# Kernel optimization log

Hardware: AMD Instinct MI355X
Metric: run time of the kernel (lower is better)

## Reference

```python
import jax, jax.numpy as jnp
import numpy as np

DIM = 512
NUM_GROUPS = 32
NUM_HEADS = 8
EPS = 1e-5


def group_norm(x, gamma, beta):
    # x: (B, C, H, W); normalize over (C//G, H, W) per group
    B, C, H, W = x.shape
    g = x.reshape(B, NUM_GROUPS, -1)
    mean = g.mean(axis=2, keepdims=True)
    var = g.var(axis=2, keepdims=True)
    g = (g - mean) * jax.lax.rsqrt(var + EPS)
    x = g.reshape(B, C, H, W)
    return x * gamma[None, :, None, None] + beta[None, :, None, None]


def setup_inputs() -> dict:
    key = jax.random.key(0)
    ks = jax.random.split(key, 7)
    B, C, H, W = 16, DIM, 32, 32
    x = jax.random.normal(ks[0], (B, C, H, W), dtype=jnp.float32)
    gamma = jnp.ones((C,), dtype=jnp.float32)
    beta = jnp.zeros((C,), dtype=jnp.float32)
    s_in = 1.0 / np.sqrt(C)
    w_qkv = jax.random.normal(ks[1], (3 * C, C), dtype=jnp.float32) * s_in
    b_qkv = jnp.zeros((3 * C,), dtype=jnp.float32)
    w_proj = jax.random.normal(ks[2], (C, C), dtype=jnp.float32) * s_in
    b_proj = jnp.zeros((C,), dtype=jnp.float32)
    return {"x": x, "gamma": gamma, "beta": beta, "w_qkv": w_qkv,
            "b_qkv": b_qkv, "w_proj": w_proj, "b_proj": b_proj}


def reference(x, gamma, beta, w_qkv, b_qkv, w_proj, b_proj):
    B, C, H, W = x.shape
    nh = NUM_HEADS
    c3 = 3 * C // nh          # per-head qkv channels (3 * head_dim)
    dh = C // nh              # head_dim
    scale = C ** (-0.5)       # NOTE: source scales by full dim, not head_dim

    h = group_norm(x, gamma, beta)

    # 1x1 conv qkv projection: (B, 3C, H, W)
    qkv = jnp.einsum('bchw,oc->bohw', h, w_qkv) + b_qkv[None, :, None, None]

    # rearrange 'b (head c) h w -> (b head) (h w) c'
    qkv = qkv.reshape(B, nh, c3, H, W)
    qkv = qkv.transpose(0, 1, 3, 4, 2).reshape(B * nh, H * W, c3)
    q, k, v = jnp.split(qkv, 3, axis=2)   # each (B*nh, HW, dh)

    score = jnp.einsum('bnc,bmc->bnm', q, k * scale)   # (B*nh, HW, HW)
    attn = jax.nn.softmax(score, axis=2)
    out = jnp.einsum('bnm,bmc->bnc', attn, v)          # (B*nh, HW, dh)

    # rearrange '(head b) (h w) c -> b (head c) h w'  (NOTE head-major, as in source)
    out = out.reshape(nh, B, H, W, dh)
    out = out.transpose(1, 0, 4, 2, 3).reshape(B, C, H, W)

    out = jnp.einsum('bchw,oc->bohw', out, w_proj) + b_proj[None, :, None, None]
    return out + x
```

## Files before the change

kernel.cpp:

```cpp
#include <hip/hip_runtime.h>
#include <stdint.h>

typedef __bf16 bf16;
typedef __attribute__((ext_vector_type(4))) float f32x4;
typedef __attribute__((ext_vector_type(8))) __bf16 bf16x8;
typedef __attribute__((ext_vector_type(4))) __bf16 bf16x4;

#define NB 16
#define CH 512
#define HWS 1024
#define NHEAD 8
#define DH 64
#define O3 1536
#define CPQ 136
#define CPF 132

#define PSW(row, col) (((row) << 6) + (((((col) >> 3) ^ ((row) & 7))) << 3) + ((col) & 7))

__device__ __forceinline__ void gload_lds16(const bf16* g, bf16* l) {
    __builtin_amdgcn_global_load_lds(
        (const __attribute__((address_space(1))) unsigned int*)g,
        (__attribute__((address_space(3))) unsigned int*)l,
        16, 0, 0);
}

#if defined(__has_builtin) && __has_builtin(__builtin_amdgcn_exp2f)
__device__ __forceinline__ float fast_exp2(float x) { return __builtin_amdgcn_exp2f(x); }
#else
__device__ __forceinline__ float fast_exp2(float x) { return exp2f(x); }
#endif

__global__ void prep(const float* __restrict__ x, float* __restrict__ stats,
                     const float* __restrict__ wq, const float* __restrict__ wp,
                     bf16* __restrict__ wq_b, bf16* __restrict__ wp_b) {
    int bx = blockIdx.x;
    if (bx < 512) {
        int b = bx >> 5, g = bx & 31;
        const float4* p = (const float4*)(x + ((size_t)(b * CH + g * 16)) * HWS);
        float s = 0.f, ss = 0.f;
        for (int i = threadIdx.x; i < 4096; i += 256) {
            float4 v = p[i];
            s  += v.x + v.y + v.z + v.w;
            ss += v.x*v.x + v.y*v.y + v.z*v.z + v.w*v.w;
        }
        for (int off = 32; off; off >>= 1) {
            s  += __shfl_xor(s,  off, 64);
            ss += __shfl_xor(ss, off, 64);
        }
        __shared__ float red[8];
        int w = threadIdx.x >> 6;
        if ((threadIdx.x & 63) == 0) { red[w*2] = s; red[w*2+1] = ss; }
        __syncthreads();
        if (threadIdx.x == 0) {
            float S  = red[0] + red[2] + red[4] + red[6];
            float SS = red[1] + red[3] + red[5] + red[7];
            float mean = S * (1.f/16384.f);
            float var  = SS * (1.f/16384.f) - mean*mean;
            stats[bx*2]   = mean;
            stats[bx*2+1] = rsqrtf(var + 1e-5f);
        }
    } else {
        int i = (bx - 512) * 256 + threadIdx.x;
        if (i < O3*CH) wq_b[i] = (bf16)wq[i];
        else           wp_b[i - O3*CH] = (bf16)wp[i - O3*CH];
    }
}

__global__ void gn_apply_t(const float* __restrict__ x, const float* __restrict__ stats,
                           const float* __restrict__ gamma, const float* __restrict__ beta,
                           bf16* __restrict__ hT) {
    __shared__ float tile[32][33];
    int bx = blockIdx.x;
    int b = bx >> 9;
    int rem = bx & 511;
    int ct = rem >> 5, nt = rem & 31;
    int tx = threadIdx.x & 31, ty = threadIdx.x >> 5;
    #pragma unroll
    for (int r = 0; r < 4; ++r) {
        int c = ct*32 + ty + r*8;
        int n = nt*32 + tx;
        float v = x[((size_t)(b * CH + c)) * HWS + n];
        int g = c >> 4;
        float mean = stats[(b*32+g)*2], rstd = stats[(b*32+g)*2+1];
        tile[ty + r*8][tx] = (v - mean) * rstd * gamma[c] + beta[c];
    }
    __syncthreads();
    #pragma unroll
    for (int r = 0; r < 4; ++r) {
        int n = nt*32 + ty + r*8;
        int c = ct*32 + tx;
        hT[((size_t)(b * HWS + n)) * CH + c] = (bf16)tile[tx][ty + r*8];
    }
}

__global__ __launch_bounds__(256, 3)
void qkv_gemm(const bf16* __restrict__ W, const bf16* __restrict__ hT,
              const float* __restrict__ bias, bf16* __restrict__ qkv,
              bf16* __restrict__ vT) {
    __shared__ __align__(16) bf16 SMEM[128*CPQ];
    bf16* As = SMEM;
    bf16* Bs = SMEM + 8192;
    int bx = blockIdx.x;
    int po = bx >> 7, qo = bx & 127;
    int obase = po*128, bnbase = qo*128;
    int tid = threadIdx.x;
    int lane = tid & 63, w = tid >> 6;
    int quad = lane >> 4, l15 = lane & 15;
    int wm = w >> 1, wn = w & 1;
    int x7 = l15 & 7;
    int srow = lane >> 3, spos = lane & 7;
    int sgc = (spos ^ srow) * 8;

    f32x4 acc[4][4] = {};
    for (int k0 = 0; k0 < 512; k0 += 64) {
        #pragma unroll
        for (int r = 0; r < 4; ++r) {
            int rb = r*32 + w*8;
            gload_lds16(W  + ((size_t)(obase  + rb + srow))*512 + k0 + sgc, &As[rb*64]);
            gload_lds16(hT + ((size_t)(bnbase + rb + srow))*512 + k0 + sgc, &Bs[rb*64]);
        }
        __syncthreads();
        #pragma unroll
        for (int ks = 0; ks < 2; ++ks) {
            int ch = (ks*4 + quad) ^ x7;
            bf16x8 af[4], bfv[4];
            #pragma unroll
            for (int mt = 0; mt < 4; ++mt)
                af[mt] = *(const bf16x8*)(&As[(wm*64 + mt*16 + l15)*64 + ch*8]);
            #pragma unroll
            for (int nt = 0; nt < 4; ++nt)
                bfv[nt] = *(const bf16x8*)(&Bs[(wn*64 + nt*16 + l15)*64 + ch*8]);
            #pragma unroll
            for (int mt = 0; mt < 4; ++mt)
                #pragma unroll
                for (int nt = 0; nt < 4; ++nt)
                    acc[mt][nt] = __builtin_amdgcn_mfma_f32_16x16x32_bf16(af[mt], bfv[nt], acc[mt][nt], 0, 0, 0);
        }
        __syncthreads();
    }

    bf16* Cs = SMEM;
    int b = bnbase >> 10;
    int nbase = bnbase & 1023;
    #pragma unroll
    for (int mt = 0; mt < 4; ++mt) {
        int o0 = obase + wm*64 + mt*16 + quad*4;
        float4 bb = *(const float4*)(bias + o0);
        int c192 = o0 % 192;
        bool isV = (c192 >= 128);
        int h = o0 / 192;
        int d0 = c192 - 128;
        #pragma unroll
        for (int nt = 0; nt < 4; ++nt) {
            int bn_l = wn*64 + nt*16 + l15;
            bf16x4 v;
            v[0] = (bf16)(acc[mt][nt][0] + bb.x);
            v[1] = (bf16)(acc[mt][nt][1] + bb.y);
            v[2] = (bf16)(acc[mt][nt][2] + bb.z);
            v[3] = (bf16)(acc[mt][nt][3] + bb.w);
            *(bf16x4*)(&Cs[bn_l*CPQ + (o0 - obase)]) = v;
            if (isV) {
                int key = nbase + bn_l;
                size_t vb_ = ((size_t)((b*8 + h)*64 + d0)) * HWS + key;
                vT[vb_]          = v[0];
                vT[vb_ + HWS]    = v[1];
                vT[vb_ + 2*HWS]  = v[2];
                vT[vb_ + 3*HWS]  = v[3];
            }
        }
    }
    __syncthreads();
    #pragma unroll
    for (int p = 0; p < 8; ++p) {
        int bn_l = p*16 + (tid >> 4);
        int o8 = (tid & 15) * 8;
        if ((obase + o8) % 192 < 128) {
            uint4 v = *(const uint4*)(&Cs[bn_l*CPQ + o8]);
            *(uint4*)(qkv + ((size_t)(bnbase + bn_l)) * O3 + obase + o8) = v;
        }
    }
}

__global__ __launch_bounds__(512, 4)
void flash_attn(const bf16* __restrict__ qkv, const bf16* __restrict__ vT,
                bf16* __restrict__ A2) {
    __shared__ __align__(16) bf16 Ks[2][64*64];
    __shared__ __align__(16) bf16 Vs[2][64*64];
    __shared__ __align__(16) bf16 Ps[8][32*64];
    int bx = blockIdx.x;
    int g = bx & 127, qt = bx >> 7;
    int b = g >> 3, h = g & 7;
    int tid = threadIdx.x, lane = tid & 63, w = tid >> 6;
    int quad = lane >> 4, l15 = lane & 15;
    int x7 = l15 & 7;
    int srow = lane >> 3, spos = lane & 7;
    int sgc = (spos ^ srow) * 8;
    const float kLog2 = 0.04419417382415922f * 1.44269504088896341f;

    bf16x8 aq[2][2];
    #pragma unroll
    for (int mt = 0; mt < 2; ++mt) {
        int qrow = qt*256 + w*32 + mt*16 + l15;
        const bf16* qb = qkv + ((size_t)(b * HWS + qrow)) * O3 + h*192;
        aq[mt][0] = *(const bf16x8*)(qb + quad*8);
        aq[mt][1] = *(const bf16x8*)(qb + 32 + quad*8);
        #pragma unroll
        for (int j = 0; j < 8; ++j) {
            aq[mt][0][j] = (bf16)((float)aq[mt][0][j] * kLog2);
            aq[mt][1][j] = (bf16)((float)aq[mt][1][j] * kLog2);
        }
    }

    const bf16* kg = qkv + ((size_t)(b*HWS + w*8 + srow))*O3 + h*192 + 64 + sgc;
    const bf16* vg = vT  + ((size_t)(g*DH  + w*8 + srow))*HWS + sgc;

    gload_lds16(kg, &Ks[0][w*512]);
    gload_lds16(vg, &Vs[0][w*512]);

    f32x4 acc[2][4] = {};
    f32x4 L4[2] = {};
    __syncthreads();

    for (int kt = 0; kt < 16; ++kt) {
        int cur = kt & 1;
        if (kt < 15) {
            gload_lds16(kg + ((size_t)((kt+1)*64))*O3, &Ks[cur^1][w*512]);
            gload_lds16(vg + (kt+1)*64,                &Vs[cur^1][w*512]);
        }
        const bf16* Kc = &Ks[cur][0];
        const bf16* Vc = &Vs[cur][0];

        #pragma unroll
        for (int nt = 0; nt < 4; ++nt) {
            bf16x8 ak0 = *(const bf16x8*)(&Kc[(nt*16 + l15)*64 + ((quad     ^ x7)*8)]);
            bf16x8 ak1 = *(const bf16x8*)(&Kc[(nt*16 + l15)*64 + (((quad+4) ^ x7)*8)]);
            #pragma unroll
            for (int mt = 0; mt < 2; ++mt) {
                f32x4 z = {};
                z = __builtin_amdgcn_mfma_f32_16x16x32_bf16(ak0, aq[mt][0], z, 0, 0, 0);
                z = __builtin_amdgcn_mfma_f32_16x16x32_bf16(ak1, aq[mt][1], z, 0, 0, 0);
                bf16x4 p;
                #pragma unroll
                for (int r = 0; r < 4; ++r) {
                    float e = fast_exp2(z[r]);
                    L4[mt][r] += e;
                    p[r] = (bf16)e;
                }
                *(bf16x4*)(&Ps[w][PSW(mt*16 + l15, nt*16 + quad*4)]) = p;
            }
        }
        bf16x8 ap[2][2];
        #pragma unroll
        for (int mt = 0; mt < 2; ++mt) {
            ap[mt][0] = *(const bf16x8*)(&Ps[w][PSW(mt*16 + l15, quad*8)]);
            ap[mt][1] = *(const bf16x8*)(&Ps[w][PSW(mt*16 + l15, 32 + quad*8)]);
        }
        #pragma unroll
        for (int dt = 0; dt < 4; ++dt) {
            bf16x8 bv0 = *(const bf16x8*)(&Vc[(dt*16 + l15)*64 + ((quad     ^ x7)*8)]);
            bf16x8 bv1 = *(const bf16x8*)(&Vc[(dt*16 + l15)*64 + (((quad+4) ^ x7)*8)]);
            #pragma unroll
            for (int mt = 0; mt < 2; ++mt) {
                acc[mt][dt] = __builtin_amdgcn_mfma_f32_16x16x32_bf16(ap[mt][0], bv0, acc[mt][dt], 0, 0, 0);
                acc[mt][dt] = __builtin_amdgcn_mfma_f32_16x16x32_bf16(ap[mt][1], bv1, acc[mt][dt], 0, 0, 0);
            }
        }
        __syncthreads();
    }

    float Linv[2][4];
    #pragma unroll
    for (int mt = 0; mt < 2; ++mt) {
        float Lf = (L4[mt][0] + L4[mt][1]) + (L4[mt][2] + L4[mt][3]);
        Lf += __shfl_xor(Lf, 16, 64);
        Lf += __shfl_xor(Lf, 32, 64);
        #pragma unroll
        for (int r = 0; r < 4; ++r)
            Linv[mt][r] = 1.f / __shfl(Lf, quad*4 + r, 64);
    }

    #pragma unroll
    for (int mt = 0; mt < 2; ++mt)
        #pragma unroll
        for (int dt = 0; dt < 4; ++dt)
            #pragma unroll
            for (int r = 0; r < 4; ++r)
                Ps[w][PSW(mt*16 + quad*4 + r, dt*16 + l15)] = (bf16)(acc[mt][dt][r] * Linv[mt][r]);

    int bp = g & 15;
    int hp = g >> 4;
    #pragma unroll
    for (int cc = 0; cc < 4; ++cc) {
        int c = cc*64 + lane;
        int row = c >> 3, dcc = c & 7;
        uint4 v = *(const uint4*)(&Ps[w][PSW(row, dcc*8)]);
        size_t idx = ((size_t)(bp * HWS + qt*256 + w*32 + row)) * CH + hp*64 + dcc*8;
        *(uint4*)(A2 + idx) = v;
    }
}

__global__ __launch_bounds__(256, 3)
void proj_gemm(const bf16* __restrict__ A2, const bf16* __restrict__ Wp,
               const float* __restrict__ bias, const float* __restrict__ x,
               float* __restrict__ out) {
    __shared__ __align__(16) bf16 SMEM[16896];
    bf16* As = SMEM;
    bf16* Bs = SMEM + 8192;
    int bx = blockIdx.x;
    int po = bx >> 7, qo = bx & 127;
    int obase = po*128, bnbase = qo*128;
    int tid = threadIdx.x;
    int lane = tid & 63, w = tid >> 6;
    int quad = lane >> 4, l15 = lane & 15;
    int wm = w >> 1, wn = w & 1;
    int x7 = l15 & 7;
    int srow = lane >> 3, spos = lane & 7;
    int sgc = (spos ^ srow) * 8;

    f32x4 acc[4][4] = {};
    for (int k0 = 0; k0 < 512; k0 += 64) {
        #pragma unroll
        for (int r = 0; r < 4; ++r) {
            int rb = r*32 + w*8;
            gload_lds16(A2 + ((size_t)(bnbase + rb + srow))*512 + k0 + sgc, &As[rb*64]);
            gload_lds16(Wp + ((size_t)(obase  + rb + srow))*512 + k0 + sgc, &Bs[rb*64]);
        }
        __syncthreads();
        #pragma unroll
        for (int ks = 0; ks < 2; ++ks) {
            int ch = (ks*4 + quad) ^ x7;
            bf16x8 af[4], bfv[4];
            #pragma unroll
            for (int mt = 0; mt < 4; ++mt)
                af[mt] = *(const bf16x8*)(&As[(wm*64 + mt*16 + l15)*64 + ch*8]);
            #pragma unroll
            for (int nt = 0; nt < 4; ++nt)
                bfv[nt] = *(const bf16x8*)(&Bs[(wn*64 + nt*16 + l15)*64 + ch*8]);
            #pragma unroll
            for (int mt = 0; mt < 4; ++mt)
                #pragma unroll
                for (int nt = 0; nt < 4; ++nt)
                    acc[mt][nt] = __builtin_amdgcn_mfma_f32_16x16x32_bf16(af[mt], bfv[nt], acc[mt][nt], 0, 0, 0);
        }
        __syncthreads();
    }

    float* Cf = (float*)SMEM;
    int bb = bnbase >> 10;
    int nbase = bnbase & 1023;
    #pragma unroll
    for (int hh = 0; hh < 2; ++hh) {
        if (wm == hh) {
            #pragma unroll
            for (int mt = 0; mt < 4; ++mt)
                #pragma unroll
                for (int nt = 0; nt < 4; ++nt)
                    #pragma unroll
                    for (int r = 0; r < 4; ++r)
                        Cf[(mt*16 + quad*4 + r)*CPF + wn*64 + nt*16 + l15] = acc[mt][nt][r];
        }
        __syncthreads();
        #pragma unroll
        for (int p = 0; p < 4; ++p) {
            int ol = p*32 + (tid >> 3);
            int nl0 = (tid & 7) * 8;
            int o = obase + ol;
            float bv = bias[o];
            #pragma unroll
            for (int jj = 0; jj < 2; ++jj) {
                int nl = nl0 + jj*4;
                size_t idx = ((size_t)(bb * CH + o)) * HWS + nbase + hh*64 + nl;
                float4 xr = *(const float4*)(x + idx);
                float4 res;
                res.x = Cf[(nl+0)*CPF + ol] + bv + xr.x;
                res.y = Cf[(nl+1)*CPF + ol] + bv + xr.y;
                res.z = Cf[(nl+2)*CPF + ol] + bv + xr.z;
                res.w = Cf[(nl+3)*CPF + ol] + bv + xr.w;
                *(float4*)(out + idx) = res;
            }
        }
        __syncthreads();
    }
}

extern "C" void kernel_launch(void* const* d_in, const int* in_sizes, int n_in,
                              void* d_out, int out_size, void* d_ws, size_t ws_size,
                              hipStream_t stream) {
    const float* x      = (const float*)d_in[0];
    const float* gamma  = (const float*)d_in[1];
    const float* beta   = (const float*)d_in[2];
    const float* w_qkv  = (const float*)d_in[3];
    const float* b_qkv  = (const float*)d_in[4];
    const float* w_proj = (const float*)d_in[5];
    const float* b_proj = (const float*)d_in[6];
    float* out = (float*)d_out;

    char* ws = (char*)d_ws;
    float* stats = (float*)(ws + 0);
    bf16*  wq_b  = (bf16*)(ws + 4096);
    bf16*  wp_b  = (bf16*)(ws + 1576960);
    bf16*  hT    = (bf16*)(ws + 2101248);
    bf16*  qkv   = (bf16*)(ws + 18878464);
    bf16*  vT    = (bf16*)(ws + 69210112);
    bf16*  A2    = hT;

    prep       <<<4608, 256, 0, stream>>>(x, stats, w_qkv, w_proj, wq_b, wp_b);
    gn_apply_t <<<8192, 256, 0, stream>>>(x, stats, gamma, beta, hT);
    qkv_gemm   <<<1536, 256, 0, stream>>>(wq_b, hT, b_qkv, qkv, vT);
    flash_attn <<<512,  512, 0, stream>>>(qkv, vT, A2);
    proj_gemm  <<<512,  256, 0, stream>>>(A2, wp_b, b_proj, x, out);
}
```

Baseline: 205.5 us.

## Load V fragments directly from global and halve flash-attention block size

The flash attention kernel now uses 256-thread blocks, each covering 128 query rows, and launches twice as many blocks. The V tile is no longer staged in shared memory; each warp loads its V MFMA operands straight from global memory into registers, split into two batches around the QK^T phase. The K prefetch for the next tile is issued after the score computation instead of at the start of the iteration. This frees LDS and may raise occupancy, but each warp now fetches V separately, which adds redundant L2 traffic and register pressure, and the later K prefetch leaves less time to overlap the load.

```diff
diff --git a/kernel.cpp b/kernel.cpp
--- a/kernel.cpp
+++ b/kernel.cpp
@@ -181,12 +181,11 @@
     }
 }
 
-__global__ __launch_bounds__(512, 4)
+__global__ __launch_bounds__(256, 4)
 void flash_attn(const bf16* __restrict__ qkv, const bf16* __restrict__ vT,
                 bf16* __restrict__ A2) {
     __shared__ __align__(16) bf16 Ks[2][64*64];
-    __shared__ __align__(16) bf16 Vs[2][64*64];
-    __shared__ __align__(16) bf16 Ps[8][32*64];
+    __shared__ __align__(16) bf16 Ps[4][32*64];
     int bx = blockIdx.x;
     int g = bx & 127, qt = bx >> 7;
     int b = g >> 3, h = g & 7;
@@ -200,7 +199,7 @@
     bf16x8 aq[2][2];
     #pragma unroll
     for (int mt = 0; mt < 2; ++mt) {
-        int qrow = qt*256 + w*32 + mt*16 + l15;
+        int qrow = qt*128 + w*32 + mt*16 + l15;
         const bf16* qb = qkv + ((size_t)(b * HWS + qrow)) * O3 + h*192;
         aq[mt][0] = *(const bf16x8*)(qb + quad*8);
         aq[mt][1] = *(const bf16x8*)(qb + 32 + quad*8);
@@ -211,24 +210,25 @@
         }
     }
 
-    const bf16* kg = qkv + ((size_t)(b*HWS + w*8 + srow))*O3 + h*192 + 64 + sgc;
-    const bf16* vg = vT  + ((size_t)(g*DH  + w*8 + srow))*HWS + sgc;
-
-    gload_lds16(kg, &Ks[0][w*512]);
-    gload_lds16(vg, &Vs[0][w*512]);
+    const bf16* kg = qkv + ((size_t)(b*HWS + w*16 + srow))*O3 + h*192 + 64 + sgc;
+    const bf16* vb0 = vT + ((size_t)(g*DH + l15))*HWS + quad*8;
+
+    gload_lds16(kg,                 &Ks[0][(w*16)*64]);
+    gload_lds16(kg + (size_t)8*O3,  &Ks[0][(w*16 + 8)*64]);
 
     f32x4 acc[2][4] = {};
     f32x4 L4[2] = {};
     __syncthreads();
 
     for (int kt = 0; kt < 16; ++kt) {
-        int cur = kt & 1;
-        if (kt < 15) {
-            gload_lds16(kg + ((size_t)((kt+1)*64))*O3, &Ks[cur^1][w*512]);
-            gload_lds16(vg + (kt+1)*64,                &Vs[cur^1][w*512]);
-        }
-        const bf16* Kc = &Ks[cur][0];
-        const bf16* Vc = &Vs[cur][0];
+        const bf16* Kc = &Ks[kt & 1][0];
+        const bf16* vkt = vb0 + kt*64;
+        bf16x8 bv[4][2];
+        #pragma unroll
+        for (int dt = 0; dt < 2; ++dt) {
+            bv[dt][0] = *(const bf16x8*)(vkt + (size_t)(dt*16)*HWS);
+            bv[dt][1] = *(const bf16x8*)(vkt + (size_t)(dt*16)*HWS + 32);
+        }
 
         #pragma unroll
         for (int nt = 0; nt < 4; ++nt) {
@@ -249,6 +249,17 @@
                 *(bf16x4*)(&Ps[w][PSW(mt*16 + l15, nt*16 + quad*4)]) = p;
             }
         }
+
+        #pragma unroll
+        for (int dt = 2; dt < 4; ++dt) {
+            bv[dt][0] = *(const bf16x8*)(vkt + (size_t)(dt*16)*HWS);
+            bv[dt][1] = *(const bf16x8*)(vkt + (size_t)(dt*16)*HWS + 32);
+        }
+        if (kt < 15) {
+            gload_lds16(kg + (size_t)((kt+1)*64)*O3,     &Ks[(kt&1)^1][(w*16)*64]);
+            gload_lds16(kg + (size_t)((kt+1)*64 + 8)*O3, &Ks[(kt&1)^1][(w*16 + 8)*64]);
+        }
+
         bf16x8 ap[2][2];
         #pragma unroll
         for (int mt = 0; mt < 2; ++mt) {
@@ -257,12 +268,10 @@
         }
         #pragma unroll
         for (int dt = 0; dt < 4; ++dt) {
-            bf16x8 bv0 = *(const bf16x8*)(&Vc[(dt*16 + l15)*64 + ((quad     ^ x7)*8)]);
-            bf16x8 bv1 = *(const bf16x8*)(&Vc[(dt*16 + l15)*64 + (((quad+4) ^ x7)*8)]);
             #pragma unroll
             for (int mt = 0; mt < 2; ++mt) {
-                acc[mt][dt] = __builtin_amdgcn_mfma_f32_16x16x32_bf16(ap[mt][0], bv0, acc[mt][dt], 0, 0, 0);
-                acc[mt][dt] = __builtin_amdgcn_mfma_f32_16x16x32_bf16(ap[mt][1], bv1, acc[mt][dt], 0, 0, 0);
+                acc[mt][dt] = __builtin_amdgcn_mfma_f32_16x16x32_bf16(ap[mt][0], bv[dt][0], acc[mt][dt], 0, 0, 0);
+                acc[mt][dt] = __builtin_amdgcn_mfma_f32_16x16x32_bf16(ap[mt][1], bv[dt][1], acc[mt][dt], 0, 0, 0);
             }
         }
         __syncthreads();
@@ -294,7 +303,7 @@
         int c = cc*64 + lane;
         int row = c >> 3, dcc = c & 7;
         uint4 v = *(const uint4*)(&Ps[w][PSW(row, dcc*8)]);
-        size_t idx = ((size_t)(bp * HWS + qt*256 + w*32 + row)) * CH + hp*64 + dcc*8;
+        size_t idx = ((size_t)(bp * HWS + qt*128 + w*32 + row)) * CH + hp*64 + dcc*8;
         *(uint4*)(A2 + idx) = v;
     }
 }
@@ -407,6 +416,6 @@
     prep       <<<4608, 256, 0, stream>>>(x, stats, w_qkv, w_proj, wq_b, wp_b);
     gn_apply_t <<<8192, 256, 0, stream>>>(x, stats, gamma, beta, hT);
     qkv_gemm   <<<1536, 256, 0, stream>>>(wq_b, hT, b_qkv, qkv, vT);
-    flash_attn <<<512,  512, 0, stream>>>(qkv, vT, A2);
+    flash_attn <<<1024, 256, 0, stream>>>(qkv, vT, A2);
     proj_gemm  <<<512,  256, 0, stream>>>(A2, wp_b, b_proj, x, out);
 }
```

New measurement: 249.3 us. 21.4% more time.

## Load V tiles directly from global into registers instead of staging through LDS

Applied to the files above, without the earlier changes.

The flash attention kernel no longer stages V tiles through double-buffered shared memory. Each wave now issues global dwordx4 loads straight into registers at the start of each key tile, and a manual vmcnt wait placed before the PV MFMAs lets those loads overlap with the QK/exp phase. This frees LDS and removes LDS write/read traffic for V, but every wave now fetches V itself, which adds redundant global/L2 traffic. The last iteration also issues an extra K prefetch that wraps around to tile 0.

```diff
diff --git a/kernel.cpp b/kernel.cpp
--- a/kernel.cpp
+++ b/kernel.cpp
@@ -3,6 +3,7 @@
 
 typedef __bf16 bf16;
 typedef __attribute__((ext_vector_type(4))) float f32x4;
+typedef __attribute__((ext_vector_type(4))) int i32x4;
 typedef __attribute__((ext_vector_type(8))) __bf16 bf16x8;
 typedef __attribute__((ext_vector_type(4))) __bf16 bf16x4;
 
@@ -22,6 +23,12 @@
         (const __attribute__((address_space(1))) unsigned int*)g,
         (__attribute__((address_space(3))) unsigned int*)l,
         16, 0, 0);
+}
+
+__device__ __forceinline__ bf16x8 gload_v4(const bf16* p) {
+    i32x4 r;
+    asm volatile("global_load_dwordx4 %0, %1, off" : "=v"(r) : "v"(p) : "memory");
+    return __builtin_bit_cast(bf16x8, r);
 }
 
 #if defined(__has_builtin) && __has_builtin(__builtin_amdgcn_exp2f)
@@ -185,7 +192,6 @@
 void flash_attn(const bf16* __restrict__ qkv, const bf16* __restrict__ vT,
                 bf16* __restrict__ A2) {
     __shared__ __align__(16) bf16 Ks[2][64*64];
-    __shared__ __align__(16) bf16 Vs[2][64*64];
     __shared__ __align__(16) bf16 Ps[8][32*64];
     int bx = blockIdx.x;
     int g = bx & 127, qt = bx >> 7;
@@ -212,10 +218,9 @@
     }
 
     const bf16* kg = qkv + ((size_t)(b*HWS + w*8 + srow))*O3 + h*192 + 64 + sgc;
-    const bf16* vg = vT  + ((size_t)(g*DH  + w*8 + srow))*HWS + sgc;
+    const bf16* vb0 = vT + ((size_t)(g*DH + l15))*HWS + quad*8;
 
     gload_lds16(kg, &Ks[0][w*512]);
-    gload_lds16(vg, &Vs[0][w*512]);
 
     f32x4 acc[2][4] = {};
     f32x4 L4[2] = {};
@@ -223,12 +228,16 @@
 
     for (int kt = 0; kt < 16; ++kt) {
         int cur = kt & 1;
-        if (kt < 15) {
-            gload_lds16(kg + ((size_t)((kt+1)*64))*O3, &Ks[cur^1][w*512]);
-            gload_lds16(vg + (kt+1)*64,                &Vs[cur^1][w*512]);
-        }
         const bf16* Kc = &Ks[cur][0];
-        const bf16* Vc = &Vs[cur][0];
+        const bf16* vkt = vb0 + kt*64;
+        bf16x8 bv[4][2];
+        #pragma unroll
+        for (int dt = 0; dt < 4; ++dt) {
+            bv[dt][0] = gload_v4(vkt + (size_t)(dt*16)*HWS);
+            bv[dt][1] = gload_v4(vkt + (size_t)(dt*16)*HWS + 32);
+        }
+        gload_lds16(kg + (size_t)(((kt+1) & 15)*64)*O3, &Ks[cur^1][w*512]);
+        __builtin_amdgcn_sched_barrier(0);
 
         #pragma unroll
         for (int nt = 0; nt < 4; ++nt) {
@@ -249,6 +258,10 @@
                 *(bf16x4*)(&Ps[w][PSW(mt*16 + l15, nt*16 + quad*4)]) = p;
             }
         }
+
+        asm volatile("s_waitcnt vmcnt(1)" ::: "memory");
+        __builtin_amdgcn_sched_barrier(0);
+
         bf16x8 ap[2][2];
         #pragma unroll
         for (int mt = 0; mt < 2; ++mt) {
@@ -257,12 +270,10 @@
         }
         #pragma unroll
         for (int dt = 0; dt < 4; ++dt) {
-            bf16x8 bv0 = *(const bf16x8*)(&Vc[(dt*16 + l15)*64 + ((quad     ^ x7)*8)]);
-            bf16x8 bv1 = *(const bf16x8*)(&Vc[(dt*16 + l15)*64 + (((quad+4) ^ x7)*8)]);
             #pragma unroll
             for (int mt = 0; mt < 2; ++mt) {
-                acc[mt][dt] = __builtin_amdgcn_mfma_f32_16x16x32_bf16(ap[mt][0], bv0, acc[mt][dt], 0, 0, 0);
-                acc[mt][dt] = __builtin_amdgcn_mfma_f32_16x16x32_bf16(ap[mt][1], bv1, acc[mt][dt], 0, 0, 0);
+                acc[mt][dt] = __builtin_amdgcn_mfma_f32_16x16x32_bf16(ap[mt][0], bv[dt][0], acc[mt][dt], 0, 0, 0);
+                acc[mt][dt] = __builtin_amdgcn_mfma_f32_16x16x32_bf16(ap[mt][1], bv[dt][1], acc[mt][dt], 0, 0, 0);
             }
         }
         __syncthreads();
```

Result: slower. 258.6 us (+25.9%).
